# Performance work log

Hardware: AMD Instinct MI355X
Metric: run time of the kernel (lower is better)

Reference implementation:

```python
import jax, jax.numpy as jnp
import numpy as np

DIM = 384
NUM_HEADS = 6
HEAD_DIM = DIM // NUM_HEADS
SCALE = HEAD_DIM ** -0.5


def setup_inputs() -> dict:
    key = jax.random.key(0)
    k_x, k_wqkv, k_bqkv, k_wp, k_bp = jax.random.split(key, 5)
    B, N, D = 16, 1024, DIM
    s = 0.02
    return {
        "x": jax.random.normal(k_x, (B, N, D), dtype=jnp.float32),
        "w_qkv": jax.random.normal(k_wqkv, (D, 3 * D), dtype=jnp.float32) * s,
        "b_qkv": jax.random.normal(k_bqkv, (3 * D,), dtype=jnp.float32) * s,
        "w_proj": jax.random.normal(k_wp, (D, D), dtype=jnp.float32) * s,
        "b_proj": jax.random.normal(k_bp, (D,), dtype=jnp.float32) * s,
    }


def reference(x, w_qkv, b_qkv, w_proj, b_proj):
    b, n, d = x.shape
    qkv = x @ w_qkv + b_qkv                               # (B, N, 3D)
    qkv = qkv.reshape(b, n, 3, NUM_HEADS, HEAD_DIM)
    qkv = jnp.transpose(qkv, (2, 0, 3, 1, 4))             # (3, B, H, N, hd)
    q, k, v = qkv[0], qkv[1], qkv[2]
    attn = jnp.einsum("bhqd,bhkd->bhqk", q, k) * SCALE    # (B, H, N, N)
    attn = jax.nn.softmax(attn, axis=-1)
    out = jnp.einsum("bhqk,bhkd->bhqd", attn, v)          # (B, H, N, hd)
    out = jnp.transpose(out, (0, 2, 1, 3)).reshape(b, n, d)
    return out @ w_proj + b_proj
```

## Files before the change

### kernel.cpp

```cpp
#include <hip/hip_runtime.h>

typedef __attribute__((ext_vector_type(8))) short short8;
typedef __attribute__((ext_vector_type(4))) float float4_t;
typedef __attribute__((ext_vector_type(4))) unsigned int uint4_t;

#define MFMA16(A, B, C) __builtin_amdgcn_mfma_f32_16x16x32_bf16(A, B, C, 0, 0, 0)

#define QSCALE 0.1803368801111168f

__device__ __forceinline__ unsigned short f2bf(float f) {
  unsigned int u = __builtin_bit_cast(unsigned int, f);
  u += 0x7FFFu + ((u >> 16) & 1u);
  return (unsigned short)(u >> 16);
}

__device__ __forceinline__ void gload16(const unsigned short* g, unsigned short* l) {
  __builtin_amdgcn_global_load_lds(
      (const __attribute__((address_space(1))) unsigned int*)(g),
      (__attribute__((address_space(3))) unsigned int*)(l), 16, 0, 0);
}

__global__ __launch_bounds__(256) void prep(
    const float* __restrict__ x, const float* __restrict__ w_qkv,
    const float* __restrict__ w_proj, unsigned short* __restrict__ xb,
    unsigned short* __restrict__ wqkvT, unsigned short* __restrict__ wprojT) {
  __shared__ unsigned short tile[32][33];
  const int bid = blockIdx.x, tid = threadIdx.x;
  if (bid < 6144) {
    const int i = bid * 256 + tid;
    float4 v = reinterpret_cast<const float4*>(x)[i];
    ushort4 r;
    r.x = f2bf(v.x); r.y = f2bf(v.y); r.z = f2bf(v.z); r.w = f2bf(v.w);
    reinterpret_cast<ushort4*>(xb)[i] = r;
    return;
  }
  const float* w; unsigned short* wT; int E, t;
  if (bid < 6576) { t = bid - 6144; w = w_qkv; wT = wqkvT; E = 1152; }
  else            { t = bid - 6576; w = w_proj; wT = wprojT; E = 384; }
  const int tiles_e = E >> 5;
  const int td = t / tiles_e, te = t - td * tiles_e;
  const int r = tid >> 3, c4 = (tid & 7) * 4;
  float4 v = *reinterpret_cast<const float4*>(&w[(size_t)(td * 32 + r) * E + te * 32 + c4]);
  tile[r][c4 + 0] = f2bf(v.x);
  tile[r][c4 + 1] = f2bf(v.y);
  tile[r][c4 + 2] = f2bf(v.z);
  tile[r][c4 + 3] = f2bf(v.w);
  __syncthreads();
  ushort4 o;
  o.x = tile[c4 + 0][r]; o.y = tile[c4 + 1][r];
  o.z = tile[c4 + 2][r]; o.w = tile[c4 + 3][r];
  *reinterpret_cast<ushort4*>(&wT[(size_t)(te * 32 + r) * 384 + td * 32 + c4]) = o;
}

__global__ __launch_bounds__(256, 3) void gemm_qkv(
    const unsigned short* __restrict__ xb,
    const unsigned short* __restrict__ wT,
    const float* __restrict__ bias,
    unsigned short* __restrict__ qb,
    unsigned short* __restrict__ kb,
    unsigned short* __restrict__ vt) {
  __shared__ alignas(16) char smem[49152];
  const int tid = threadIdx.x;
  const int wg = (blockIdx.x & 7) * 288 + (blockIdx.x >> 3);
  const int bm = wg / 18, bn = wg - bm * 18;
  const int m0 = bm * 128, n0 = bn * 64;
  const int lane = tid & 63, wid = tid >> 6;
  const int lr = lane & 15, lg = lane >> 4;
  const int wm = wid >> 1, wn = wid & 1;
  float4_t acc[4][2] = {};

  const unsigned short* asrc[4];
  const unsigned short* bsrc[2];
  int adst[4], bdst[2];
#pragma unroll
  for (int i = 0; i < 4; ++i) {
    const int idx = tid + i * 256;
    const int r = idx >> 3, c8 = idx & 7;
    asrc[i] = xb + (size_t)(m0 + r) * 384 + (c8 ^ (r & 7)) * 8;
    adst[i] = idx * 16;
  }
#pragma unroll
  for (int i = 0; i < 2; ++i) {
    const int idx = tid + i * 256;
    const int r = idx >> 3, c8 = idx & 7;
    bsrc[i] = wT + (size_t)(n0 + r) * 384 + (c8 ^ (r & 7)) * 8;
    bdst[i] = idx * 16;
  }
  const int rxor = (lr & 7) << 4;

#pragma unroll
  for (int i = 0; i < 4; ++i) gload16(asrc[i], (unsigned short*)(smem + adst[i]));
#pragma unroll
  for (int i = 0; i < 2; ++i) gload16(bsrc[i], (unsigned short*)(smem + 32768 + bdst[i]));
  __syncthreads();

#pragma unroll
  for (int kt = 0; kt < 6; ++kt) {
    const int cur = kt & 1;
    if (kt < 5) {
#pragma unroll
      for (int i = 0; i < 4; ++i)
        gload16(asrc[i] + (kt + 1) * 64,
                (unsigned short*)(smem + (cur ^ 1) * 16384 + adst[i]));
#pragma unroll
      for (int i = 0; i < 2; ++i)
        gload16(bsrc[i] + (kt + 1) * 64,
                (unsigned short*)(smem + 32768 + (cur ^ 1) * 8192 + bdst[i]));
    }
    const char* Ab = smem + cur * 16384;
    const char* Bb = smem + 32768 + cur * 8192;
#pragma unroll
    for (int kk = 0; kk < 2; ++kk) {
      short8 a[4], b[2];
#pragma unroll
      for (int f = 0; f < 4; ++f)
        a[f] = *reinterpret_cast<const short8*>(
            Ab + (wm * 64 + f * 16 + lr) * 128 + ((kk * 64 + lg * 16) ^ rxor));
#pragma unroll
      for (int f = 0; f < 2; ++f)
        b[f] = *reinterpret_cast<const short8*>(
            Bb + (wn * 32 + f * 16 + lr) * 128 + ((kk * 64 + lg * 16) ^ rxor));
      if (bn < 12) {
#pragma unroll
        for (int mf = 0; mf < 4; ++mf)
#pragma unroll
          for (int nf = 0; nf < 2; ++nf)
            acc[mf][nf] = MFMA16(b[nf], a[mf], acc[mf][nf]);
      } else {
#pragma unroll
        for (int mf = 0; mf < 4; ++mf)
#pragma unroll
          for (int nf = 0; nf < 2; ++nf)
            acc[mf][nf] = MFMA16(a[mf], b[nf], acc[mf][nf]);
      }
    }
    __syncthreads();
  }

  if (bn < 12) {
    const int whichk = (bn >= 6);
    unsigned short* dst = whichk ? kb : qb;
    const float sc = whichk ? 1.f : QSCALE;
#pragma unroll
    for (int nf = 0; nf < 2; ++nf) {
      const int e0 = n0 + wn * 32 + nf * 16 + lg * 4;
      const int d0 = e0 - whichk * 384;
      const int h = d0 >> 6, hi0 = d0 & 63;
      const float4 bv4 = *reinterpret_cast<const float4*>(&bias[e0]);
#pragma unroll
      for (int mf = 0; mf < 4; ++mf) {
        const int mm = m0 + wm * 64 + mf * 16 + lr;
        const int b0 = mm >> 10, n_b = mm & 1023;
        const size_t bhh = (size_t)(b0 * 6 + h);
        ushort4 sv;
        sv.x = f2bf((acc[mf][nf][0] + bv4.x) * sc);
        sv.y = f2bf((acc[mf][nf][1] + bv4.y) * sc);
        sv.z = f2bf((acc[mf][nf][2] + bv4.z) * sc);
        sv.w = f2bf((acc[mf][nf][3] + bv4.w) * sc);
        *reinterpret_cast<ushort4*>(&dst[bhh * 65536 + (size_t)n_b * 64 + hi0]) = sv;
      }
    }
  } else {
#pragma unroll
    for (int nf = 0; nf < 2; ++nf) {
      const int e = n0 + wn * 32 + nf * 16 + lr;
      const float bv = bias[e];
      const int d = e - 768;
      const int h = d >> 6, hi = d & 63;
#pragma unroll
      for (int mf = 0; mf < 4; ++mf) {
        const int mm0 = m0 + wm * 64 + mf * 16 + lg * 4;
        const int b0 = mm0 >> 10, n_b = mm0 & 1023;
        const size_t bhh = (size_t)(b0 * 6 + h);
        const int np = (n_b & ~31) | ((n_b & 12) << 1) | ((n_b & 16) >> 2);
        ushort4 sv;
        sv.x = f2bf(acc[mf][nf][0] + bv);
        sv.y = f2bf(acc[mf][nf][1] + bv);
        sv.z = f2bf(acc[mf][nf][2] + bv);
        sv.w = f2bf(acc[mf][nf][3] + bv);
        *reinterpret_cast<ushort4*>(&vt[bhh * 65536 + (size_t)hi * 1024 + np]) = sv;
      }
    }
  }
}

__global__ __launch_bounds__(256, 3) void attn(
    const unsigned short* __restrict__ qb,
    const unsigned short* __restrict__ kb,
    const unsigned short* __restrict__ vt,
    unsigned short* __restrict__ ab) {
  __shared__ alignas(16) char smem[32768];
  const int tid = threadIdx.x;
  const int wg = (blockIdx.x & 7) * 96 + (blockIdx.x >> 3);
  const int bh = wg >> 3, qt = wg & 7;
  const int lane = tid & 63, wid = tid >> 6;
  const int lr = lane & 15, lg = lane >> 4;
  const size_t base = (size_t)bh * 65536;
  const unsigned short* qp = qb + base;
  const unsigned short* kp = kb + base;
  const unsigned short* vp = vt + base;
  const int q0 = qt * 128 + wid * 32;

  short8 aq[2][2];
#pragma unroll
  for (int qf = 0; qf < 2; ++qf)
#pragma unroll
    for (int h = 0; h < 2; ++h)
      aq[qf][h] = *reinterpret_cast<const short8*>(
          &qp[(size_t)(q0 + qf * 16 + lr) * 64 + h * 32 + lg * 8]);

  const unsigned short* ksrc[2];
  const unsigned short* vsrc[2];
  int soff[2];
#pragma unroll
  for (int i = 0; i < 2; ++i) {
    const int idx = tid + i * 256;
    const int r = idx >> 3, c8 = idx & 7;
    const int cc = (c8 ^ (r & 7)) * 8;
    ksrc[i] = kp + r * 64 + cc;
    vsrc[i] = vp + r * 1024 + cc;
    soff[i] = idx * 16;
  }
  const int xr = (lr & 7) << 4;

  float lsum0 = 0.f, lsum1 = 0.f;
  float4_t o0[4] = {}, o1[4] = {};

#pragma unroll
  for (int i = 0; i < 2; ++i) {
    gload16(ksrc[i], (unsigned short*)(smem + soff[i]));
    gload16(vsrc[i], (unsigned short*)(smem + 16384 + soff[i]));
  }
  __syncthreads();

  for (int kt = 0; kt < 16; ++kt) {
    const int cur = kt & 1;
    if (kt < 15) {
      const int nb = (cur ^ 1) * 8192;
#pragma unroll
      for (int i = 0; i < 2; ++i) {
        gload16(ksrc[i] + (kt + 1) * 4096, (unsigned short*)(smem + nb + soff[i]));
        gload16(vsrc[i] + (kt + 1) * 64, (unsigned short*)(smem + 16384 + nb + soff[i]));
      }
    }
    const char* kbase = smem + cur * 8192;
    const char* vbase = smem + 16384 + cur * 8192;

#pragma unroll
    for (int half = 0; half < 2; ++half) {
      short8 bk00 = *reinterpret_cast<const short8*>(
          kbase + (half * 32 + lr) * 128 + ((lg * 16) ^ xr));
      short8 bk01 = *reinterpret_cast<const short8*>(
          kbase + (half * 32 + lr) * 128 + ((64 + lg * 16) ^ xr));
      short8 bk10 = *reinterpret_cast<const short8*>(
          kbase + (half * 32 + 16 + lr) * 128 + ((lg * 16) ^ xr));
      short8 bk11 = *reinterpret_cast<const short8*>(
          kbase + (half * 32 + 16 + lr) * 128 + ((64 + lg * 16) ^ xr));
      short8 bv0 = *reinterpret_cast<const short8*>(
          vbase + (0 * 16 + lr) * 128 + ((half * 64 + lg * 16) ^ xr));
      short8 bv1 = *reinterpret_cast<const short8*>(
          vbase + (1 * 16 + lr) * 128 + ((half * 64 + lg * 16) ^ xr));
      short8 bv2 = *reinterpret_cast<const short8*>(
          vbase + (2 * 16 + lr) * 128 + ((half * 64 + lg * 16) ^ xr));
      short8 bv3 = *reinterpret_cast<const short8*>(
          vbase + (3 * 16 + lr) * 128 + ((half * 64 + lg * 16) ^ xr));

#pragma unroll
      for (int qf = 0; qf < 2; ++qf) {
        float4_t s0 = {}, s1 = {};
        __builtin_amdgcn_s_setprio(1);
        s0 = MFMA16(bk00, aq[qf][0], s0);
        s0 = MFMA16(bk01, aq[qf][1], s0);
        s1 = MFMA16(bk10, aq[qf][0], s1);
        s1 = MFMA16(bk11, aq[qf][1], s1);
        __builtin_amdgcn_s_setprio(0);

        unsigned int dw0, dw1, dw2, dw3;
        {
          const float p0 = __builtin_amdgcn_exp2f(s0[0]);
          const float p1 = __builtin_amdgcn_exp2f(s0[1]);
          const float p2 = __builtin_amdgcn_exp2f(s0[2]);
          const float p3 = __builtin_amdgcn_exp2f(s0[3]);
          asm("v_cvt_pk_bf16_f32 %0, %1, %2" : "=v"(dw0) : "v"(p0), "v"(p1));
          asm("v_cvt_pk_bf16_f32 %0, %1, %2" : "=v"(dw1) : "v"(p2), "v"(p3));
          const float p4 = __builtin_amdgcn_exp2f(s1[0]);
          const float p5 = __builtin_amdgcn_exp2f(s1[1]);
          const float p6 = __builtin_amdgcn_exp2f(s1[2]);
          const float p7 = __builtin_amdgcn_exp2f(s1[3]);
          asm("v_cvt_pk_bf16_f32 %0, %1, %2" : "=v"(dw2) : "v"(p4), "v"(p5));
          asm("v_cvt_pk_bf16_f32 %0, %1, %2" : "=v"(dw3) : "v"(p6), "v"(p7));
        }
        const float t0 = __builtin_bit_cast(float, dw0 << 16) +
                         __builtin_bit_cast(float, dw0 & 0xFFFF0000u);
        const float t1 = __builtin_bit_cast(float, dw1 << 16) +
                         __builtin_bit_cast(float, dw1 & 0xFFFF0000u);
        const float t2 = __builtin_bit_cast(float, dw2 << 16) +
                         __builtin_bit_cast(float, dw2 & 0xFFFF0000u);
        const float t3 = __builtin_bit_cast(float, dw3 << 16) +
                         __builtin_bit_cast(float, dw3 & 0xFFFF0000u);
        if (qf == 0) lsum0 += (t0 + t1) + (t2 + t3);
        else         lsum1 += (t0 + t1) + (t2 + t3);

        uint4_t pw;
        pw[0] = dw0; pw[1] = dw1; pw[2] = dw2; pw[3] = dw3;
        const short8 pa = __builtin_bit_cast(short8, pw);
        float4_t* o = (qf == 0) ? o0 : o1;
        __builtin_amdgcn_s_setprio(1);
        o[0] = MFMA16(pa, bv0, o[0]);
        o[1] = MFMA16(pa, bv1, o[1]);
        o[2] = MFMA16(pa, bv2, o[2]);
        o[3] = MFMA16(pa, bv3, o[3]);
        __builtin_amdgcn_s_setprio(0);
      }
    }
    __syncthreads();
  }

  float ti0 = lsum0, ti1 = lsum1;
  ti0 += __shfl_xor(ti0, 16);
  ti0 += __shfl_xor(ti0, 32);
  ti1 += __shfl_xor(ti1, 16);
  ti1 += __shfl_xor(ti1, 32);
  const float inv0 = 1.f / ti0;
  const float inv1 = 1.f / ti1;

  const int b = bh / 6, h = bh - b * 6;
#pragma unroll
  for (int qf = 0; qf < 2; ++qf) {
    const float4_t* o = (qf == 0) ? o0 : o1;
    const float inv = (qf == 0) ? inv0 : inv1;
    float invj[4];
#pragma unroll
    for (int j = 0; j < 4; ++j)
      invj[j] = __shfl(inv, lg * 4 + j);
#pragma unroll
    for (int f = 0; f < 4; ++f)
#pragma unroll
      for (int j = 0; j < 4; ++j) {
        const int q = q0 + qf * 16 + lg * 4 + j;
        ab[(size_t)(b * 1024 + q) * 384 + h * 64 + f * 16 + lr] =
            f2bf(o[f][j] * invj[j]);
      }
  }
}

__global__ __launch_bounds__(256, 3) void gemm_proj(
    const unsigned short* __restrict__ ab,
    const unsigned short* __restrict__ wT,
    const float* __restrict__ bias,
    float* __restrict__ out) {
  __shared__ alignas(16) char smem[49152];
  const int tid = threadIdx.x;
  const int wg = (blockIdx.x & 7) * 96 + (blockIdx.x >> 3);
  const int bm = wg / 3, bn = wg - bm * 3;
  const int m0 = bm * 64, n0 = bn * 128;
  const int lane = tid & 63, wid = tid >> 6;
  const int lr = lane & 15, lg = lane >> 4;
  const int wm = wid >> 1, wn = wid & 1;
  float4_t acc[2][4] = {};

  const unsigned short* asrc[2];
  const unsigned short* bsrc[4];
  int adst[2], bdst[4];
#pragma unroll
  for (int i = 0; i < 2; ++i) {
    const int idx = tid + i * 256;
    const int r = idx >> 3, c8 = idx & 7;
    asrc[i] = ab + (size_t)(m0 + r) * 384 + (c8 ^ (r & 7)) * 8;
    adst[i] = idx * 16;
  }
#pragma unroll
  for (int i = 0; i < 4; ++i) {
    const int idx = tid + i * 256;
    const int r = idx >> 3, c8 = idx & 7;
    bsrc[i] = wT + (size_t)(n0 + r) * 384 + (c8 ^ (r & 7)) * 8;
    bdst[i] = idx * 16;
  }
  const int rxor = (lr & 7) << 4;

#pragma unroll
  for (int i = 0; i < 2; ++i) gload16(asrc[i], (unsigned short*)(smem + adst[i]));
#pragma unroll
  for (int i = 0; i < 4; ++i) gload16(bsrc[i], (unsigned short*)(smem + 16384 + bdst[i]));
  __syncthreads();

#pragma unroll
  for (int kt = 0; kt < 6; ++kt) {
    const int cur = kt & 1;
    if (kt < 5) {
#pragma unroll
      for (int i = 0; i < 2; ++i)
        gload16(asrc[i] + (kt + 1) * 64, (unsigned short*)(smem + (cur ^ 1) * 8192 + adst[i]));
#pragma unroll
      for (int i = 0; i < 4; ++i)
        gload16(bsrc[i] + (kt + 1) * 64, (unsigned short*)(smem + 16384 + (cur ^ 1) * 16384 + bdst[i]));
    }
    const char* Ab = smem + cur * 8192;
    const char* Bb = smem + 16384 + cur * 16384;
#pragma unroll
    for (int kk = 0; kk < 2; ++kk) {
      short8 a[2], b[4];
#pragma unroll
      for (int f = 0; f < 2; ++f)
        a[f] = *reinterpret_cast<const short8*>(
            Ab + (wm * 32 + f * 16 + lr) * 128 + ((kk * 64 + lg * 16) ^ rxor));
#pragma unroll
      for (int f = 0; f < 4; ++f)
        b[f] = *reinterpret_cast<const short8*>(
            Bb + (wn * 64 + f * 16 + lr) * 128 + ((kk * 64 + lg * 16) ^ rxor));
#pragma unroll
      for (int mf = 0; mf < 2; ++mf)
#pragma unroll
        for (int nf = 0; nf < 4; ++nf)
          acc[mf][nf] = MFMA16(b[nf], a[mf], acc[mf][nf]);
    }
    __syncthreads();
  }

#pragma unroll
  for (int nf = 0; nf < 4; ++nf) {
    const int e0 = n0 + wn * 64 + nf * 16 + lg * 4;
    const float4 bv4 = *reinterpret_cast<const float4*>(&bias[e0]);
#pragma unroll
    for (int mf = 0; mf < 2; ++mf) {
      const int mm = m0 + wm * 32 + mf * 16 + lr;
      float4 ov;
      ov.x = acc[mf][nf][0] + bv4.x;
      ov.y = acc[mf][nf][1] + bv4.y;
      ov.z = acc[mf][nf][2] + bv4.z;
      ov.w = acc[mf][nf][3] + bv4.w;
      *reinterpret_cast<float4*>(&out[(size_t)mm * 384 + e0]) = ov;
    }
  }
}

extern "C" void kernel_launch(void* const* d_in, const int* in_sizes, int n_in,
                              void* d_out, int out_size, void* d_ws, size_t ws_size,
                              hipStream_t stream) {
  const float* x      = (const float*)d_in[0];
  const float* w_qkv  = (const float*)d_in[1];
  const float* b_qkv  = (const float*)d_in[2];
  const float* w_proj = (const float*)d_in[3];
  const float* b_proj = (const float*)d_in[4];
  float* out = (float*)d_out;

  char* ws = (char*)d_ws;
  unsigned short* xb     = (unsigned short*)(ws);
  unsigned short* wqkvT  = (unsigned short*)(ws + 12582912);
  unsigned short* wprojT = (unsigned short*)(ws + 13467648);
  unsigned short* qb     = (unsigned short*)(ws + 13762560);
  unsigned short* kb     = (unsigned short*)(ws + 26345472);
  unsigned short* vt     = (unsigned short*)(ws + 38928384);
  unsigned short* ab     = xb;

  prep<<<6720, 256, 0, stream>>>(x, w_qkv, w_proj, xb, wqkvT, wprojT);
  gemm_qkv<<<2304, 256, 0, stream>>>(xb, wqkvT, b_qkv, qb, kb, vt);
  attn<<<768, 256, 0, stream>>>(qb, kb, vt, ab);
  gemm_proj<<<768, 256, 0, stream>>>(ab, wprojT, b_proj, out);
}
```

Measured before the change: 85.92 us.

## Fuse fp32-to-bf16 conversion of x into QKV GEMM A-tile loads

Removes the separate pass that converted x to bf16 in the prep kernel, so prep now only transposes the weights. The QKV GEMM instead reads fp32 x into registers, converts to bf16 and writes the swizzled tile to LDS after the MFMA stage, replacing the direct global-to-LDS loads for A. This avoids writing and re-reading a 12 MB bf16 copy of x. In exchange, x is reread in fp32 by each of the 18 column blocks, which doubles A-side global traffic, and register pressure rises under the 3-blocks-per-CU launch bound.

Result: slower. 92.98 us (+8.2%).

```diff
diff --git a/kernel.cpp b/kernel.cpp
--- a/kernel.cpp
+++ b/kernel.cpp
@@ -21,22 +21,13 @@
 }
 
 __global__ __launch_bounds__(256) void prep(
-    const float* __restrict__ x, const float* __restrict__ w_qkv,
-    const float* __restrict__ w_proj, unsigned short* __restrict__ xb,
+    const float* __restrict__ w_qkv, const float* __restrict__ w_proj,
     unsigned short* __restrict__ wqkvT, unsigned short* __restrict__ wprojT) {
   __shared__ unsigned short tile[32][33];
   const int bid = blockIdx.x, tid = threadIdx.x;
-  if (bid < 6144) {
-    const int i = bid * 256 + tid;
-    float4 v = reinterpret_cast<const float4*>(x)[i];
-    ushort4 r;
-    r.x = f2bf(v.x); r.y = f2bf(v.y); r.z = f2bf(v.z); r.w = f2bf(v.w);
-    reinterpret_cast<ushort4*>(xb)[i] = r;
-    return;
-  }
   const float* w; unsigned short* wT; int E, t;
-  if (bid < 6576) { t = bid - 6144; w = w_qkv; wT = wqkvT; E = 1152; }
-  else            { t = bid - 6576; w = w_proj; wT = wprojT; E = 384; }
+  if (bid < 432) { t = bid; w = w_qkv; wT = wqkvT; E = 1152; }
+  else           { t = bid - 432; w = w_proj; wT = wprojT; E = 384; }
   const int tiles_e = E >> 5;
   const int td = t / tiles_e, te = t - td * tiles_e;
   const int r = tid >> 3, c4 = (tid & 7) * 4;
@@ -53,7 +44,7 @@
 }
 
 __global__ __launch_bounds__(256, 3) void gemm_qkv(
-    const unsigned short* __restrict__ xb,
+    const float* __restrict__ x,
     const unsigned short* __restrict__ wT,
     const float* __restrict__ bias,
     unsigned short* __restrict__ qb,
@@ -69,14 +60,14 @@
   const int wm = wid >> 1, wn = wid & 1;
   float4_t acc[4][2] = {};
 
-  const unsigned short* asrc[4];
+  const float* xsrc[4];
   const unsigned short* bsrc[2];
   int adst[4], bdst[2];
 #pragma unroll
   for (int i = 0; i < 4; ++i) {
     const int idx = tid + i * 256;
     const int r = idx >> 3, c8 = idx & 7;
-    asrc[i] = xb + (size_t)(m0 + r) * 384 + (c8 ^ (r & 7)) * 8;
+    xsrc[i] = x + (size_t)(m0 + r) * 384 + (c8 ^ (r & 7)) * 8;
     adst[i] = idx * 16;
   }
 #pragma unroll
@@ -88,20 +79,37 @@
   }
   const int rxor = (lr & 7) << 4;
 
-#pragma unroll
-  for (int i = 0; i < 4; ++i) gload16(asrc[i], (unsigned short*)(smem + adst[i]));
+  float4 av[4][2];
+  auto loadA = [&](int kt) {
+#pragma unroll
+    for (int i = 0; i < 4; ++i) {
+      av[i][0] = *reinterpret_cast<const float4*>(xsrc[i] + kt * 64);
+      av[i][1] = *reinterpret_cast<const float4*>(xsrc[i] + kt * 64 + 4);
+    }
+  };
+  auto cvtWriteA = [&](char* abuf) {
+#pragma unroll
+    for (int i = 0; i < 4; ++i) {
+      uint4_t u;
+      u[0] = (unsigned int)f2bf(av[i][0].x) | ((unsigned int)f2bf(av[i][0].y) << 16);
+      u[1] = (unsigned int)f2bf(av[i][0].z) | ((unsigned int)f2bf(av[i][0].w) << 16);
+      u[2] = (unsigned int)f2bf(av[i][1].x) | ((unsigned int)f2bf(av[i][1].y) << 16);
+      u[3] = (unsigned int)f2bf(av[i][1].z) | ((unsigned int)f2bf(av[i][1].w) << 16);
+      *reinterpret_cast<uint4_t*>(abuf + adst[i]) = u;
+    }
+  };
+
+  loadA(0);
 #pragma unroll
   for (int i = 0; i < 2; ++i) gload16(bsrc[i], (unsigned short*)(smem + 32768 + bdst[i]));
+  cvtWriteA(smem);
   __syncthreads();
 
 #pragma unroll
   for (int kt = 0; kt < 6; ++kt) {
     const int cur = kt & 1;
     if (kt < 5) {
-#pragma unroll
-      for (int i = 0; i < 4; ++i)
-        gload16(asrc[i] + (kt + 1) * 64,
-                (unsigned short*)(smem + (cur ^ 1) * 16384 + adst[i]));
+      loadA(kt + 1);
 #pragma unroll
       for (int i = 0; i < 2; ++i)
         gload16(bsrc[i] + (kt + 1) * 64,
@@ -134,6 +142,7 @@
             acc[mf][nf] = MFMA16(a[mf], b[nf], acc[mf][nf]);
       }
     }
+    if (kt < 5) cvtWriteA(smem + (cur ^ 1) * 16384);
     __syncthreads();
   }
 
@@ -445,16 +454,15 @@
   float* out = (float*)d_out;
 
   char* ws = (char*)d_ws;
-  unsigned short* xb     = (unsigned short*)(ws);
+  unsigned short* ab     = (unsigned short*)(ws);
   unsigned short* wqkvT  = (unsigned short*)(ws + 12582912);
   unsigned short* wprojT = (unsigned short*)(ws + 13467648);
   unsigned short* qb     = (unsigned short*)(ws + 13762560);
   unsigned short* kb     = (unsigned short*)(ws + 26345472);
   unsigned short* vt     = (unsigned short*)(ws + 38928384);
-  unsigned short* ab     = xb;
-
-  prep<<<6720, 256, 0, stream>>>(x, w_qkv, w_proj, xb, wqkvT, wprojT);
-  gemm_qkv<<<2304, 256, 0, stream>>>(xb, wqkvT, b_qkv, qb, kb, vt);
+
+  prep<<<576, 256, 0, stream>>>(w_qkv, w_proj, wqkvT, wprojT);
+  gemm_qkv<<<2304, 256, 0, stream>>>(x, wqkvT, b_qkv, qb, kb, vt);
   attn<<<768, 256, 0, stream>>>(qb, kb, vt, ab);
   gemm_proj<<<768, 256, 0, stream>>>(ab, wprojT, b_proj, out);
 }
```

## Triple-buffer K/V tiles in attention with explicit vmcnt waits

Applied to the files above, without the earlier changes.

Moves the attention kernel's K/V staging from double to triple buffering in LDS, raising shared memory to 48KB. Loads are issued two tiles ahead, and partial s_waitcnt vmcnt counts let the kernel wait only for the tile it is about to use instead of draining every outstanding load. The goal is to hide more global-load latency behind the MFMA work. In exchange the larger LDS footprint may reduce how many workgroups fit per CU (launch bounds request 3), and the hand-counted vmcnt values must match the number of loads actually in flight.

After: 87.21 us. No clear change (+1.5%).

```diff
diff --git a/kernel.cpp b/kernel.cpp
--- a/kernel.cpp
+++ b/kernel.cpp
@@ -189,7 +189,7 @@
     const unsigned short* __restrict__ kb,
     const unsigned short* __restrict__ vt,
     unsigned short* __restrict__ ab) {
-  __shared__ alignas(16) char smem[32768];
+  __shared__ alignas(16) char smem[49152];
   const int tid = threadIdx.x;
   const int wg = (blockIdx.x & 7) * 96 + (blockIdx.x >> 3);
   const int bh = wg >> 3, qt = wg & 7;
@@ -226,25 +226,35 @@
   float lsum0 = 0.f, lsum1 = 0.f;
   float4_t o0[4] = {}, o1[4] = {};
 
-#pragma unroll
-  for (int i = 0; i < 2; ++i) {
-    gload16(ksrc[i], (unsigned short*)(smem + soff[i]));
-    gload16(vsrc[i], (unsigned short*)(smem + 16384 + soff[i]));
-  }
-  __syncthreads();
-
+  auto stage = [&](int kt, int b) {
+#pragma unroll
+    for (int i = 0; i < 2; ++i) {
+      gload16(ksrc[i] + kt * 4096, (unsigned short*)(smem + b * 8192 + soff[i]));
+      gload16(vsrc[i] + kt * 64, (unsigned short*)(smem + 24576 + b * 8192 + soff[i]));
+    }
+  };
+
+  stage(0, 0);
+  stage(1, 1);
+  asm volatile("s_waitcnt vmcnt(4)" ::: "memory");
+  __builtin_amdgcn_sched_barrier(0);
+  __builtin_amdgcn_s_barrier();
+
+  int cb = 0, sb = 2;
   for (int kt = 0; kt < 16; ++kt) {
-    const int cur = kt & 1;
-    if (kt < 15) {
-      const int nb = (cur ^ 1) * 8192;
-#pragma unroll
-      for (int i = 0; i < 2; ++i) {
-        gload16(ksrc[i] + (kt + 1) * 4096, (unsigned short*)(smem + nb + soff[i]));
-        gload16(vsrc[i] + (kt + 1) * 64, (unsigned short*)(smem + 16384 + nb + soff[i]));
-      }
-    }
-    const char* kbase = smem + cur * 8192;
-    const char* vbase = smem + 16384 + cur * 8192;
+    if (kt < 14) {
+      stage(kt + 2, sb);
+      asm volatile("s_waitcnt vmcnt(8)" ::: "memory");
+    } else if (kt == 14) {
+      asm volatile("s_waitcnt vmcnt(4)" ::: "memory");
+    } else {
+      asm volatile("s_waitcnt vmcnt(0)" ::: "memory");
+    }
+    __builtin_amdgcn_sched_barrier(0);
+    __builtin_amdgcn_s_barrier();
+
+    const char* kbase = smem + cb * 8192;
+    const char* vbase = smem + 24576 + cb * 8192;
 
 #pragma unroll
     for (int half = 0; half < 2; ++half) {
@@ -313,7 +323,9 @@
         __builtin_amdgcn_s_setprio(0);
       }
     }
-    __syncthreads();
+    __builtin_amdgcn_s_barrier();
+    cb = (cb == 2) ? 0 : cb + 1;
+    sb = (sb == 2) ? 0 : sb + 1;
   }
 
   float ti0 = lsum0, ti1 = lsum1;
```
